# Optimization experiments

Measured on AMD Instinct MI355X. Metric: run time of the kernel, lower is better.

Reference implementation:

```python
import jax, jax.numpy as jnp
import numpy as np

DIM = 1024
HEADS = 16
HEAD_DIM = DIM // HEADS
B, N = 8, 1024


def setup_inputs() -> dict:
    key = jax.random.key(0)
    ks = jax.random.split(key, 10)
    s = lambda fan_in: 1.0 / np.sqrt(fan_in)
    return {
        "x": jax.random.normal(ks[0], (B, N, DIM), jnp.float32),
        "pose_angles": jax.random.normal(ks[1], (B, 3), jnp.float32),
        # weights stored (in, out) so y = x @ W + b (equivalent to torch Linear)
        "Wqkv": jax.random.normal(ks[2], (DIM, 3 * DIM), jnp.float32) * s(DIM),
        "bqkv": jnp.zeros((3 * DIM,), jnp.float32),
        "W1": jax.random.normal(ks[3], (3, 64), jnp.float32) * s(3),
        "b1": jnp.zeros((64,), jnp.float32),
        "W2": jax.random.normal(ks[4], (64, 3 * DIM), jnp.float32) * s(64),
        "b2": jnp.zeros((3 * DIM,), jnp.float32),
        "Wproj": jax.random.normal(ks[5], (DIM, DIM), jnp.float32) * s(DIM),
        "bproj": jnp.zeros((DIM,), jnp.float32),
    }


def reference(x, pose_angles, Wqkv, bqkv, W1, b1, W2, b2, Wproj, bproj):
    Bq, Nq, C = x.shape
    H, D = HEADS, HEAD_DIM
    # qkv projection -> [B,N,3,H,D] -> [3,B,H,N,D]
    qkv = (x @ Wqkv + bqkv).reshape(Bq, Nq, 3, H, D).transpose(2, 0, 3, 1, 4)
    q, k, v = qkv[0], qkv[1], qkv[2]
    # pose MLP: 3 -> 64 -> 3*dim, chunked into per-head biases [B,H,1,D]
    pose_emb = jax.nn.relu(pose_angles @ W1 + b1) @ W2 + b2
    pose_q, pose_k, pose_v = jnp.split(pose_emb, 3, axis=1)
    pose_q = pose_q.reshape(Bq, H, 1, D)
    pose_k = pose_k.reshape(Bq, H, 1, D)
    pose_v = pose_v.reshape(Bq, H, 1, D)
    q = q + pose_q
    k = k + pose_k
    v = v + pose_v
    scale = 1.0 / jnp.sqrt(jnp.asarray(D, x.dtype))
    attn = jax.nn.softmax(jnp.einsum("bhnd,bhmd->bhnm", q, k) * scale, axis=-1)
    # dropout is identity in eval mode
    out = jnp.einsum("bhnm,bhmd->bhnd", attn, v)
    out = out.transpose(0, 2, 1, 3).reshape(Bq, Nq, C)
    return out @ Wproj + bproj
```

## Files before the change

### kernel.cpp

```cpp
#include <hip/hip_runtime.h>
#include <stdint.h>

typedef unsigned short u16;
typedef short bf16x8 __attribute__((ext_vector_type(8)));
typedef short bf16x4 __attribute__((ext_vector_type(4)));
typedef float f32x4 __attribute__((ext_vector_type(4)));
typedef u16 u16x4 __attribute__((ext_vector_type(4)));

__device__ __forceinline__ u16 f2bf(float f) {
  union { float f; unsigned int u; } v; v.f = f;
  unsigned int r = v.u + 0x7fffu + ((v.u >> 16) & 1u);
  return (u16)(r >> 16);
}

__device__ __forceinline__ void async16(const void* g, void* l) {
  __builtin_amdgcn_global_load_lds(
      (const __attribute__((address_space(1))) unsigned int*)g,
      (__attribute__((address_space(3))) unsigned int*)l, 16, 0, 0);
}

__device__ __forceinline__ f32x4 mfma16x16(bf16x4 a, bf16x4 b, f32x4 c) {
#if __has_builtin(__builtin_amdgcn_mfma_f32_16x16x16bf16_1k)
  return __builtin_amdgcn_mfma_f32_16x16x16bf16_1k(a, b, c, 0, 0, 0);
#else
  asm volatile("v_mfma_f32_16x16x16_bf16 %0, %1, %2, %0\n\ts_nop 7\n\ts_nop 7"
               : "+v"(c) : "v"(a), "v"(b));
  return c;
#endif
}

__global__ void pose_mlp_kernel(const float* __restrict__ ang, const float* __restrict__ W1,
                                const float* __restrict__ b1, const float* __restrict__ W2,
                                const float* __restrict__ b2, float* __restrict__ pose) {
  __shared__ float hid[8][64];
  int t = threadIdx.x;
  for (int idx = t; idx < 512; idx += 256) {
    int b = idx >> 6, j = idx & 63;
    float a = b1[j];
#pragma unroll
    for (int i = 0; i < 3; ++i) a += ang[b * 3 + i] * W1[i * 64 + j];
    hid[b][j] = fmaxf(a, 0.f);
  }
  __syncthreads();
  int idx = blockIdx.x * 256 + t;
  int b = idx / 3072, c = idx - b * 3072;
  float a = b2[c];
#pragma unroll
  for (int j = 0; j < 64; ++j) a += hid[b][j] * W2[j * 3072 + c];
  pose[idx] = a;
}

__global__ void cast_x_kernel(const float4* __restrict__ x, u16x4* __restrict__ y, int n4) {
  int i = blockIdx.x * blockDim.x + threadIdx.x;
  const int stride = gridDim.x * blockDim.x;
  for (; i < n4; i += stride) {
    float4 v = x[i];
    u16x4 o;
    o[0] = f2bf(v.x); o[1] = f2bf(v.y); o[2] = f2bf(v.z); o[3] = f2bf(v.w);
    y[i] = o;
  }
}

__global__ void transpose_cast_kernel(const float* __restrict__ W, u16* __restrict__ Wt,
                                      int Kdim, int Ncol) {
  __shared__ float tile[64][65];
  const int tx = threadIdx.x, ty = threadIdx.y;
  const int c0 = blockIdx.x * 64, k0 = blockIdx.y * 64;
#pragma unroll
  for (int rr = 0; rr < 16; ++rr) {
    int row = rr * 4 + ty;
    tile[row][tx] = W[(size_t)(k0 + row) * Ncol + c0 + tx];
  }
  __syncthreads();
#pragma unroll
  for (int rr = 0; rr < 16; ++rr) {
    int row = rr * 4 + ty;
    Wt[(size_t)(c0 + row) * Kdim + k0 + tx] = f2bf(tile[tx][row]);
  }
}

template <int EPI>
__global__ void __launch_bounds__(512) gemm8_kernel(
    const u16* __restrict__ A, const u16* __restrict__ Bt,
    const float* __restrict__ bias, const float* __restrict__ pose,
    u16* __restrict__ qout, u16* __restrict__ kout, u16* __restrict__ vtout,
    float* __restrict__ cout, int Kdim, int Ncols, int nTilesX) {
  constexpr int BOFF = 256 * 64;
  __shared__ u16 lds[2][(256 + 128) * 64];
  const int t = threadIdx.x, l = t & 63, w = t >> 6;
  const int g = l >> 4, r16 = l & 15;
  const int wr = w >> 1, wc = w & 1;
  const int xk = r16 & 7;
  const int nwg = gridDim.x, cpx = nwg >> 3;
  const int swz = (blockIdx.x & 7) * cpx + (blockIdx.x >> 3);
  const int n0 = (swz % nTilesX) * 128, m0 = (swz / nTilesX) * 256;
  const u16* Ab = A + (size_t)m0 * Kdim;
  const u16* Bb = Bt + (size_t)n0 * Kdim;

  auto stage = [&](int buf, int kt, int st) {
#pragma unroll
    for (int it = 0; it < 2; ++it) {
      int idx = it * 512 + t, row = idx >> 3;
      int seg = (idx & 7) ^ (row & 7);
      if (st < 2)
        async16(Ab + (size_t)(st * 128 + row) * Kdim + kt + seg * 8,
                &lds[buf][st * 128 * 64 + idx * 8]);
      else
        async16(Bb + (size_t)row * Kdim + kt + seg * 8, &lds[buf][BOFF + idx * 8]);
    }
  };

  f32x4 acc[4][4] = {};
  const int nT = Kdim >> 6;
#pragma unroll
  for (int st = 0; st < 3; ++st) stage(0, 0, st);

  for (int tt = 0; tt < nT; ++tt) {
    const int cur = tt & 1, nxt = cur ^ 1;
    const bool pf = (tt + 1 < nT);
    const int ktn = (tt + 1) << 6;
    if (pf) {
      stage(nxt, ktn, 0);
      __builtin_amdgcn_sched_barrier(0);
      asm volatile("s_waitcnt vmcnt(2)" ::: "memory");
    } else {
      asm volatile("s_waitcnt vmcnt(0)" ::: "memory");
    }
    __builtin_amdgcn_s_barrier();
    __builtin_amdgcn_sched_barrier(0);
    bf16x8 bfr[4][2], af[2][2];
#pragma unroll
    for (int nj = 0; nj < 4; ++nj)
#pragma unroll
      for (int ks = 0; ks < 2; ++ks)
        bfr[nj][ks] = *(const bf16x8*)&lds[cur][BOFF + (wc * 64 + nj * 16 + r16) * 64 +
                                               ((ks * 4 + g) ^ xk) * 8];
#pragma unroll
    for (int mi = 0; mi < 2; ++mi)
#pragma unroll
      for (int ks = 0; ks < 2; ++ks)
        af[mi][ks] = *(const bf16x8*)&lds[cur][(wr * 64 + mi * 16 + r16) * 64 +
                                              ((ks * 4 + g) ^ xk) * 8];
    __builtin_amdgcn_s_setprio(1);
#pragma unroll
    for (int ks = 0; ks < 2; ++ks)
#pragma unroll
      for (int mi = 0; mi < 2; ++mi)
#pragma unroll
        for (int nj = 0; nj < 4; ++nj)
          acc[mi][nj] = __builtin_amdgcn_mfma_f32_16x16x32_bf16(af[mi][ks], bfr[nj][ks],
                                                                acc[mi][nj], 0, 0, 0);
    __builtin_amdgcn_s_setprio(0);
    if (pf) { stage(nxt, ktn, 1); stage(nxt, ktn, 2); }
    bf16x8 af2[2][2];
#pragma unroll
    for (int mi = 0; mi < 2; ++mi)
#pragma unroll
      for (int ks = 0; ks < 2; ++ks)
        af2[mi][ks] = *(const bf16x8*)&lds[cur][(wr * 64 + (mi + 2) * 16 + r16) * 64 +
                                               ((ks * 4 + g) ^ xk) * 8];
    __builtin_amdgcn_s_setprio(1);
#pragma unroll
    for (int ks = 0; ks < 2; ++ks)
#pragma unroll
      for (int mi = 0; mi < 2; ++mi)
#pragma unroll
        for (int nj = 0; nj < 4; ++nj)
          acc[mi + 2][nj] = __builtin_amdgcn_mfma_f32_16x16x32_bf16(af2[mi][ks], bfr[nj][ks],
                                                                    acc[mi + 2][nj], 0, 0, 0);
    __builtin_amdgcn_s_setprio(0);
    __builtin_amdgcn_s_barrier();
  }

#pragma unroll
  for (int mi = 0; mi < 4; ++mi)
#pragma unroll
    for (int nj = 0; nj < 4; ++nj)
#pragma unroll
      for (int r = 0; r < 4; ++r) {
        int row = m0 + wr * 64 + mi * 16 + g * 4 + r;
        int col = n0 + wc * 64 + nj * 16 + r16;
        float v = acc[mi][nj][r] + bias[col];
        if (EPI == 0) {
          int b = row >> 10, n = row & 1023;
          v += pose[b * 3072 + col];
          u16 hv = f2bf(v);
          int three = col >> 10, hh = (col >> 6) & 15, d = col & 63;
          size_t bhh = (size_t)(b * 16 + hh);
          if (three == 0)      qout[(bhh * 1024 + n) * 64 + d] = hv;
          else if (three == 1) kout[(bhh * 1024 + n) * 64 + d] = hv;
          else                 vtout[(bhh * 64 + d) * 1024 + n] = hv;
        } else {
          cout[(size_t)row * Ncols + col] = v;
        }
      }
}

__global__ void __launch_bounds__(256) attn_kernel(
    const u16* __restrict__ Qb, const u16* __restrict__ Kb,
    const u16* __restrict__ Vtb, u16* __restrict__ aout) {
  __shared__ u16 ldsK[64][72];
  __shared__ u16 ldsV[64][72];
  const int t = threadIdx.x, l = t & 63, w = t >> 6;
  const int g = l >> 4, r16 = l & 15;
  const int bh = blockIdx.x >> 4, qt = blockIdx.x & 15;
  const int b = bh >> 4, h = bh & 15;
  const int q0 = qt * 64 + w * 16;
  const u16* Qp = Qb + ((size_t)bh * 1024 + q0 + r16) * 64;
  bf16x8 qreg0 = *(const bf16x8*)(Qp + g * 8);
  bf16x8 qreg1 = *(const bf16x8*)(Qp + 32 + g * 8);
  const u16* Kbase = Kb + (size_t)bh * 1024 * 64;
  const u16* Vbase = Vtb + (size_t)bh * 64 * 1024;
  float m = -1e30f, rs = 0.f;
  f32x4 o[4] = {};
  for (int key0 = 0; key0 < 1024; key0 += 64) {
#pragma unroll
    for (int ii = 0; ii < 2; ++ii) {
      int idx = ii * 256 + t, row = idx >> 3, seg = idx & 7;
      *(bf16x8*)&ldsK[row][seg * 8] = *(const bf16x8*)(Kbase + (size_t)(key0 + row) * 64 + seg * 8);
      *(bf16x8*)&ldsV[row][seg * 8] = *(const bf16x8*)(Vbase + (size_t)row * 1024 + key0 + seg * 8);
    }
    __syncthreads();
    f32x4 s[4] = {};
#pragma unroll
    for (int f = 0; f < 4; ++f) {
      bf16x8 ak0 = *(const bf16x8*)&ldsK[f * 16 + r16][g * 8];
      s[f] = __builtin_amdgcn_mfma_f32_16x16x32_bf16(ak0, qreg0, s[f], 0, 0, 0);
      bf16x8 ak1 = *(const bf16x8*)&ldsK[f * 16 + r16][32 + g * 8];
      s[f] = __builtin_amdgcn_mfma_f32_16x16x32_bf16(ak1, qreg1, s[f], 0, 0, 0);
    }
    float mt = -1e30f;
#pragma unroll
    for (int f = 0; f < 4; ++f)
#pragma unroll
      for (int r = 0; r < 4; ++r) { s[f][r] *= 0.125f; mt = fmaxf(mt, s[f][r]); }
    mt = fmaxf(mt, __shfl_xor(mt, 16));
    mt = fmaxf(mt, __shfl_xor(mt, 32));
    float mnew = fmaxf(m, mt);
    float alpha = __expf(m - mnew);
    float rt = 0.f;
    bf16x4 pa[4];
#pragma unroll
    for (int f = 0; f < 4; ++f) {
#pragma unroll
      for (int r = 0; r < 4; ++r) {
        float p = __expf(s[f][r] - mnew);
        rt += p;
        pa[f][r] = (short)f2bf(p);
      }
    }
    rt += __shfl_xor(rt, 16);
    rt += __shfl_xor(rt, 32);
    rs = rs * alpha + rt;
    m = mnew;
    float ar[4];
#pragma unroll
    for (int r = 0; r < 4; ++r) ar[r] = __shfl(alpha, (l & 48) | (g * 4 + r));
#pragma unroll
    for (int nf = 0; nf < 4; ++nf)
#pragma unroll
      for (int r = 0; r < 4; ++r) o[nf][r] *= ar[r];
#pragma unroll
    for (int s4 = 0; s4 < 4; ++s4)
#pragma unroll
      for (int nf = 0; nf < 4; ++nf) {
        bf16x4 bv = *(const bf16x4*)&ldsV[nf * 16 + r16][s4 * 16 + g * 4];
        o[nf] = mfma16x16(pa[s4], bv, o[nf]);
      }
    __syncthreads();
  }
  float rr[4];
#pragma unroll
  for (int r = 0; r < 4; ++r) rr[r] = __shfl(1.0f / rs, (l & 48) | (g * 4 + r));
#pragma unroll
  for (int nf = 0; nf < 4; ++nf)
#pragma unroll
    for (int r = 0; r < 4; ++r) {
      int qq = qt * 64 + w * 16 + g * 4 + r;
      int d = nf * 16 + r16;
      aout[((size_t)b * 1024 + qq) * 1024 + h * 64 + d] = f2bf(o[nf][r] * rr[r]);
    }
}

extern "C" void kernel_launch(void* const* d_in, const int* in_sizes, int n_in,
                              void* d_out, int out_size, void* d_ws, size_t ws_size,
                              hipStream_t stream) {
  (void)in_sizes; (void)n_in; (void)out_size; (void)ws_size;
  const float* x     = (const float*)d_in[0];
  const float* ang   = (const float*)d_in[1];
  const float* Wqkv  = (const float*)d_in[2];
  const float* bqkv  = (const float*)d_in[3];
  const float* W1    = (const float*)d_in[4];
  const float* b1    = (const float*)d_in[5];
  const float* W2    = (const float*)d_in[6];
  const float* b2    = (const float*)d_in[7];
  const float* Wproj = (const float*)d_in[8];
  const float* bproj = (const float*)d_in[9];
  float* out = (float*)d_out;
  char* ws = (char*)d_ws;

  u16* xh     = (u16*)(ws);
  u16* wqkvt  = (u16*)(ws + (size_t)16 * 1024 * 1024);
  u16* wprojt = (u16*)(ws + (size_t)22 * 1024 * 1024);
  float* pose = (float*)(ws + (size_t)24 * 1024 * 1024);
  u16* Qb     = (u16*)(ws + (size_t)25 * 1024 * 1024);
  u16* Kb     = (u16*)(ws + (size_t)41 * 1024 * 1024);
  u16* Vtb    = (u16*)(ws + (size_t)57 * 1024 * 1024);

  pose_mlp_kernel<<<96, 256, 0, stream>>>(ang, W1, b1, W2, b2, pose);
  cast_x_kernel<<<2048, 256, 0, stream>>>((const float4*)x, (u16x4*)xh, 8 * 1024 * 1024 / 4);
  transpose_cast_kernel<<<dim3(48, 16), dim3(64, 4), 0, stream>>>(Wqkv, wqkvt, 1024, 3072);
  transpose_cast_kernel<<<dim3(16, 16), dim3(64, 4), 0, stream>>>(Wproj, wprojt, 1024, 1024);
  gemm8_kernel<0><<<768, 512, 0, stream>>>(xh, wqkvt, bqkv, pose,
                                           Qb, Kb, Vtb, nullptr, 1024, 3072, 24);
  attn_kernel<<<2048, 256, 0, stream>>>(Qb, Kb, Vtb, xh);
  gemm8_kernel<1><<<256, 512, 0, stream>>>(xh, wprojt, bproj, nullptr,
                                           nullptr, nullptr, nullptr, out, 1024, 1024, 8);
}
```

Before: 207.8 us.

## Triple-buffer GEMM LDS staging to prefetch two K-tiles ahead

Changes the GEMM main loop from double to triple buffering in LDS, issuing async global-to-LDS loads two K-steps ahead and rotating three slots. The vmcnt waits are retuned so each step waits only for the tile it consumes, giving loads more latency slack. In exchange, LDS use grows to 3x48KB = 144KB per block, which lowers occupancy to a single 512-thread block per CU and depends on the vmcnt counts being exactly right.

```diff
diff --git a/kernel.cpp b/kernel.cpp
--- a/kernel.cpp
+++ b/kernel.cpp
@@ -86,7 +86,8 @@
     u16* __restrict__ qout, u16* __restrict__ kout, u16* __restrict__ vtout,
     float* __restrict__ cout, int Kdim, int Ncols, int nTilesX) {
   constexpr int BOFF = 256 * 64;
-  __shared__ u16 lds[2][(256 + 128) * 64];
+  constexpr int SLOT = (256 + 128) * 64;
+  __shared__ u16 lds[3][SLOT];
   const int t = threadIdx.x, l = t & 63, w = t >> 6;
   const int g = l >> 4, r16 = l & 15;
   const int wr = w >> 1, wc = w & 1;
@@ -97,16 +98,16 @@
   const u16* Ab = A + (size_t)m0 * Kdim;
   const u16* Bb = Bt + (size_t)n0 * Kdim;
 
-  auto stage = [&](int buf, int kt, int st) {
+  auto stage = [&](int slot, int kt, int st) {
 #pragma unroll
     for (int it = 0; it < 2; ++it) {
       int idx = it * 512 + t, row = idx >> 3;
       int seg = (idx & 7) ^ (row & 7);
       if (st < 2)
         async16(Ab + (size_t)(st * 128 + row) * Kdim + kt + seg * 8,
-                &lds[buf][st * 128 * 64 + idx * 8]);
+                &lds[slot][st * 128 * 64 + idx * 8]);
       else
-        async16(Bb + (size_t)row * Kdim + kt + seg * 8, &lds[buf][BOFF + idx * 8]);
+        async16(Bb + (size_t)row * Kdim + kt + seg * 8, &lds[slot][BOFF + idx * 8]);
     }
   };
 
@@ -114,33 +115,34 @@
   const int nT = Kdim >> 6;
 #pragma unroll
   for (int st = 0; st < 3; ++st) stage(0, 0, st);
-
+#pragma unroll
+  for (int st = 0; st < 3; ++st) stage(1, 64, st);
+
+  int s0 = 0, s1 = 1, s2 = 2;
   for (int tt = 0; tt < nT; ++tt) {
-    const int cur = tt & 1, nxt = cur ^ 1;
-    const bool pf = (tt + 1 < nT);
-    const int ktn = (tt + 1) << 6;
-    if (pf) {
-      stage(nxt, ktn, 0);
-      __builtin_amdgcn_sched_barrier(0);
-      asm volatile("s_waitcnt vmcnt(2)" ::: "memory");
-    } else {
-      asm volatile("s_waitcnt vmcnt(0)" ::: "memory");
-    }
+    const bool pf = (tt + 2 < nT);
+    const int ktn = (tt + 2) << 6;
+    if (pf) stage(s2, ktn, 0);
+    __builtin_amdgcn_sched_barrier(0);
+    if (pf)                asm volatile("s_waitcnt vmcnt(8)" ::: "memory");
+    else if (tt + 1 < nT)  asm volatile("s_waitcnt vmcnt(6)" ::: "memory");
+    else                   asm volatile("s_waitcnt vmcnt(0)" ::: "memory");
     __builtin_amdgcn_s_barrier();
     __builtin_amdgcn_sched_barrier(0);
+    const u16* L = lds[s0];
     bf16x8 bfr[4][2], af[2][2];
 #pragma unroll
     for (int nj = 0; nj < 4; ++nj)
 #pragma unroll
       for (int ks = 0; ks < 2; ++ks)
-        bfr[nj][ks] = *(const bf16x8*)&lds[cur][BOFF + (wc * 64 + nj * 16 + r16) * 64 +
-                                               ((ks * 4 + g) ^ xk) * 8];
+        bfr[nj][ks] = *(const bf16x8*)&L[BOFF + (wc * 64 + nj * 16 + r16) * 64 +
+                                        ((ks * 4 + g) ^ xk) * 8];
 #pragma unroll
     for (int mi = 0; mi < 2; ++mi)
 #pragma unroll
       for (int ks = 0; ks < 2; ++ks)
-        af[mi][ks] = *(const bf16x8*)&lds[cur][(wr * 64 + mi * 16 + r16) * 64 +
-                                              ((ks * 4 + g) ^ xk) * 8];
+        af[mi][ks] = *(const bf16x8*)&L[(wr * 64 + mi * 16 + r16) * 64 +
+                                       ((ks * 4 + g) ^ xk) * 8];
     __builtin_amdgcn_s_setprio(1);
 #pragma unroll
     for (int ks = 0; ks < 2; ++ks)
@@ -151,14 +153,14 @@
           acc[mi][nj] = __builtin_amdgcn_mfma_f32_16x16x32_bf16(af[mi][ks], bfr[nj][ks],
                                                                 acc[mi][nj], 0, 0, 0);
     __builtin_amdgcn_s_setprio(0);
-    if (pf) { stage(nxt, ktn, 1); stage(nxt, ktn, 2); }
+    if (pf) { stage(s2, ktn, 1); stage(s2, ktn, 2); }
     bf16x8 af2[2][2];
 #pragma unroll
     for (int mi = 0; mi < 2; ++mi)
 #pragma unroll
       for (int ks = 0; ks < 2; ++ks)
-        af2[mi][ks] = *(const bf16x8*)&lds[cur][(wr * 64 + (mi + 2) * 16 + r16) * 64 +
-                                               ((ks * 4 + g) ^ xk) * 8];
+        af2[mi][ks] = *(const bf16x8*)&L[(wr * 64 + (mi + 2) * 16 + r16) * 64 +
+                                        ((ks * 4 + g) ^ xk) * 8];
     __builtin_amdgcn_s_setprio(1);
 #pragma unroll
     for (int ks = 0; ks < 2; ++ks)
@@ -170,6 +172,8 @@
                                                                     acc[mi + 2][nj], 0, 0, 0);
     __builtin_amdgcn_s_setprio(0);
     __builtin_amdgcn_s_barrier();
+    __builtin_amdgcn_sched_barrier(0);
+    int tmp = s0; s0 = s1; s1 = s2; s2 = tmp;
   }
 
 #pragma unroll
```

New measurement: 210.0 us. No clear change (+1.0%).

## Merge preprocessing kernels into one launch and reorder attention block mapping

Applied to the files above, without the earlier changes.

Four preprocessing kernels (pose MLP, x cast to bf16, and two weight transpose-casts) are combined into a single front_kernel whose blocks branch on blockIdx ranges. This removes three kernel launches and the gaps between them, and lets the independent jobs run concurrently. The attention grid mapping also changes so that consecutive blocks cover different batch-heads for the same query tile instead of the same head, which spreads K/V reads across heads. The fused kernel uses the largest shared-memory footprint for all blocks, which may reduce occupancy for the cast blocks.

```diff
diff --git a/kernel.cpp b/kernel.cpp
--- a/kernel.cpp
+++ b/kernel.cpp
@@ -29,53 +29,61 @@
 #endif
 }
 
-__global__ void pose_mlp_kernel(const float* __restrict__ ang, const float* __restrict__ W1,
-                                const float* __restrict__ b1, const float* __restrict__ W2,
-                                const float* __restrict__ b2, float* __restrict__ pose) {
-  __shared__ float hid[8][64];
-  int t = threadIdx.x;
-  for (int idx = t; idx < 512; idx += 256) {
-    int b = idx >> 6, j = idx & 63;
-    float a = b1[j];
-#pragma unroll
-    for (int i = 0; i < 3; ++i) a += ang[b * 3 + i] * W1[i * 64 + j];
-    hid[b][j] = fmaxf(a, 0.f);
-  }
-  __syncthreads();
-  int idx = blockIdx.x * 256 + t;
-  int b = idx / 3072, c = idx - b * 3072;
-  float a = b2[c];
-#pragma unroll
-  for (int j = 0; j < 64; ++j) a += hid[b][j] * W2[j * 3072 + c];
-  pose[idx] = a;
-}
-
-__global__ void cast_x_kernel(const float4* __restrict__ x, u16x4* __restrict__ y, int n4) {
-  int i = blockIdx.x * blockDim.x + threadIdx.x;
-  const int stride = gridDim.x * blockDim.x;
-  for (; i < n4; i += stride) {
-    float4 v = x[i];
-    u16x4 o;
-    o[0] = f2bf(v.x); o[1] = f2bf(v.y); o[2] = f2bf(v.z); o[3] = f2bf(v.w);
-    y[i] = o;
-  }
-}
-
-__global__ void transpose_cast_kernel(const float* __restrict__ W, u16* __restrict__ Wt,
-                                      int Kdim, int Ncol) {
-  __shared__ float tile[64][65];
-  const int tx = threadIdx.x, ty = threadIdx.y;
-  const int c0 = blockIdx.x * 64, k0 = blockIdx.y * 64;
-#pragma unroll
-  for (int rr = 0; rr < 16; ++rr) {
-    int row = rr * 4 + ty;
-    tile[row][tx] = W[(size_t)(k0 + row) * Ncol + c0 + tx];
-  }
-  __syncthreads();
-#pragma unroll
-  for (int rr = 0; rr < 16; ++rr) {
-    int row = rr * 4 + ty;
-    Wt[(size_t)(c0 + row) * Kdim + k0 + tx] = f2bf(tile[tx][row]);
+__global__ void __launch_bounds__(256) front_kernel(
+    const float4* __restrict__ x4, u16x4* __restrict__ xh4,
+    const float* __restrict__ ang, const float* __restrict__ W1,
+    const float* __restrict__ b1, const float* __restrict__ W2,
+    const float* __restrict__ b2, float* __restrict__ pose,
+    const float* __restrict__ Wqkv, u16* __restrict__ wqkvt,
+    const float* __restrict__ Wproj, u16* __restrict__ wprojt) {
+  __shared__ float sh[64 * 65];
+  const int fb = blockIdx.x, t = threadIdx.x;
+  if (fb < 96) {
+    float (*hid)[64] = (float (*)[64])sh;
+    for (int idx = t; idx < 512; idx += 256) {
+      int b = idx >> 6, j = idx & 63;
+      float a = b1[j];
+#pragma unroll
+      for (int i = 0; i < 3; ++i) a += ang[b * 3 + i] * W1[i * 64 + j];
+      hid[b][j] = fmaxf(a, 0.f);
+    }
+    __syncthreads();
+    int idx = fb * 256 + t;
+    int b = idx / 3072, c = idx - b * 3072;
+    float a = b2[c];
+#pragma unroll
+    for (int j = 0; j < 64; ++j) a += hid[b][j] * W2[j * 3072 + c];
+    pose[idx] = a;
+  } else if (fb < 1120) {
+    const int n4 = 8 * 1024 * 1024 / 4;
+    int i = (fb - 96) * 256 + t;
+    const int stride = 1024 * 256;
+    for (; i < n4; i += stride) {
+      float4 v = x4[i];
+      u16x4 o;
+      o[0] = f2bf(v.x); o[1] = f2bf(v.y); o[2] = f2bf(v.z); o[3] = f2bf(v.w);
+      xh4[i] = o;
+    }
+  } else {
+    const float* W; u16* Wt; int Kdim, Ncol, bx, by;
+    if (fb < 1888) { W = Wqkv; Wt = wqkvt; Kdim = 1024; Ncol = 3072;
+                     int b = fb - 1120; bx = b % 48; by = b / 48; }
+    else           { W = Wproj; Wt = wprojt; Kdim = 1024; Ncol = 1024;
+                     int b = fb - 1888; bx = b % 16; by = b / 16; }
+    float (*tile)[65] = (float (*)[65])sh;
+    const int tx = t & 63, ty = t >> 6;
+    const int c0 = bx * 64, k0 = by * 64;
+#pragma unroll
+    for (int rr = 0; rr < 16; ++rr) {
+      int row = rr * 4 + ty;
+      tile[row][tx] = W[(size_t)(k0 + row) * Ncol + c0 + tx];
+    }
+    __syncthreads();
+#pragma unroll
+    for (int rr = 0; rr < 16; ++rr) {
+      int row = rr * 4 + ty;
+      Wt[(size_t)(c0 + row) * Kdim + k0 + tx] = f2bf(tile[tx][row]);
+    }
   }
 }
 
@@ -203,7 +211,8 @@
   __shared__ u16 ldsV[64][72];
   const int t = threadIdx.x, l = t & 63, w = t >> 6;
   const int g = l >> 4, r16 = l & 15;
-  const int bh = blockIdx.x >> 4, qt = blockIdx.x & 15;
+  const int blk = blockIdx.x;
+  const int bh = blk & 127, qt = blk >> 7;
   const int b = bh >> 4, h = bh & 15;
   const int q0 = qt * 64 + w * 16;
   const u16* Qp = Qb + ((size_t)bh * 1024 + q0 + r16) * 64;
@@ -307,10 +316,9 @@
   u16* Kb     = (u16*)(ws + (size_t)41 * 1024 * 1024);
   u16* Vtb    = (u16*)(ws + (size_t)57 * 1024 * 1024);
 
-  pose_mlp_kernel<<<96, 256, 0, stream>>>(ang, W1, b1, W2, b2, pose);
-  cast_x_kernel<<<2048, 256, 0, stream>>>((const float4*)x, (u16x4*)xh, 8 * 1024 * 1024 / 4);
-  transpose_cast_kernel<<<dim3(48, 16), dim3(64, 4), 0, stream>>>(Wqkv, wqkvt, 1024, 3072);
-  transpose_cast_kernel<<<dim3(16, 16), dim3(64, 4), 0, stream>>>(Wproj, wprojt, 1024, 1024);
+  front_kernel<<<2144, 256, 0, stream>>>((const float4*)x, (u16x4*)xh,
+                                         ang, W1, b1, W2, b2, pose,
+                                         Wqkv, wqkvt, Wproj, wprojt);
   gemm8_kernel<0><<<768, 512, 0, stream>>>(xh, wqkvt, bqkv, pose,
                                            Qb, Kb, Vtb, nullptr, 1024, 3072, 24);
   attn_kernel<<<2048, 256, 0, stream>>>(Qb, Kb, Vtb, xh);
```

New measurement: 198.0 us. 4.7% less time.
